# Kernel tuning notes

Hardware: AMD Instinct MI355X
Metric: run time of the kernel (lower is better)

Reference implementation:

```python
import jax, jax.numpy as jnp
import numpy as np

HEADS, OUT_CH = 8, 32  # GATConv(128, 256//8, heads=8) -> concat width 256
NEG_SLOPE = 0.2


def setup_inputs() -> dict:
    key = jax.random.key(0)
    ks = jax.random.split(key, 12)
    N, E, F_IN = 50000, 500000, 128
    H, C = HEADS, OUT_CH
    HID = H * C            # 256
    x = jax.random.normal(ks[0], (N, F_IN), dtype=jnp.float32)
    edge_index = jax.random.randint(ks[1], (2, E), 0, N, dtype=jnp.int64)
    s = 1.0 / np.sqrt(F_IN)
    W_gat = jax.random.normal(ks[2], (F_IN, H * C), dtype=jnp.float32) * s
    att_src = jax.random.normal(ks[3], (H, C), dtype=jnp.float32) * (1.0 / np.sqrt(C))
    att_dst = jax.random.normal(ks[4], (H, C), dtype=jnp.float32) * (1.0 / np.sqrt(C))
    b_gat = jnp.zeros((HID,), dtype=jnp.float32)
    W1 = jax.random.normal(ks[5], (HID, HID // 2), dtype=jnp.float32) * (1.0 / np.sqrt(HID))
    b1 = jnp.zeros((HID // 2,), dtype=jnp.float32)
    W2 = jax.random.normal(ks[6], (HID // 2, 6), dtype=jnp.float32) * (1.0 / np.sqrt(HID // 2))
    b2 = jnp.zeros((6,), dtype=jnp.float32)
    return {"x": x, "edge_index": edge_index, "W_gat": W_gat, "att_src": att_src,
            "att_dst": att_dst, "b_gat": b_gat, "W1": W1, "b1": b1, "W2": W2, "b2": b2}


def _gat_forward(x, edge_index, W_gat, att_src, att_dst, b_gat):
    N = x.shape[0]
    H, C = HEADS, OUT_CH
    # add self loops (PyG GATConv default)
    loop = jnp.arange(N, dtype=edge_index.dtype)
    src = jnp.concatenate([edge_index[0], loop])
    dst = jnp.concatenate([edge_index[1], loop])
    # per-node transform: [N, H, C]
    xh = (x @ W_gat).reshape(N, H, C)
    a_src = jnp.einsum('nhc,hc->nh', xh, att_src)  # [N, H]
    a_dst = jnp.einsum('nhc,hc->nh', xh, att_dst)  # [N, H]
    alpha = a_src[src] + a_dst[dst]                # [Etot, H]
    alpha = jnp.where(alpha >= 0, alpha, NEG_SLOPE * alpha)  # leaky relu
    # segment softmax over destination nodes
    m = jax.ops.segment_max(alpha, dst, num_segments=N)     # [N, H]
    m = jax.lax.stop_gradient(m)
    ex = jnp.exp(alpha - m[dst])
    denom = jax.ops.segment_sum(ex, dst, num_segments=N)    # [N, H]
    coef = ex / denom[dst]                                   # [Etot, H]
    # weighted scatter-add aggregation
    msgs = xh[src] * coef[:, :, None]                        # [Etot, H, C]
    out = jax.ops.segment_sum(msgs, dst, num_segments=N)     # [N, H, C]
    return out.reshape(N, H * C) + b_gat


def reference(x, edge_index, W_gat, att_src, att_dst, b_gat, W1, b1, W2, b2):
    h = _gat_forward(x, edge_index, W_gat, att_src, att_dst, b_gat)
    h = jax.nn.elu(h)
    g = jnp.mean(h, axis=0, keepdims=True)   # [1, 256] mean pool
    g = jax.nn.relu(g @ W1 + b1)
    return g @ W2 + b2                        # [1, 6] logits
```

## Files before the change

### kernel.cpp

```cpp
#include <hip/hip_runtime.h>
#include <hip/hip_fp8.h>
#include <math.h>

#define F_IN 128
#define HID 256
#define NH 8
#define CAP 40
#define BCAP 4096

typedef _Float16 h16;
typedef __attribute__((ext_vector_type(8))) _Float16 half8;
typedef __attribute__((ext_vector_type(4))) float f32x4;

__device__ inline unsigned char f32_to_fp8(float v) {
#if __has_builtin(__builtin_amdgcn_cvt_pk_fp8_f32)
    return (unsigned char)(__builtin_amdgcn_cvt_pk_fp8_f32(v, v, 0, false) & 0xff);
#else
    __hip_fp8_e4m3 t(v);
    return (unsigned char)t.__x;
#endif
}

__device__ inline void fp8x4_to_f32(int w, float* out) {
#if __has_builtin(__builtin_amdgcn_cvt_pk_f32_fp8)
    auto lo = __builtin_amdgcn_cvt_pk_f32_fp8(w, false);
    auto hi = __builtin_amdgcn_cvt_pk_f32_fp8(w, true);
    out[0] = lo[0]; out[1] = lo[1]; out[2] = hi[0]; out[3] = hi[1];
#else
    #pragma unroll
    for (int k = 0; k < 4; ++k) {
        __hip_fp8_e4m3 t;
        t.__x = (unsigned char)((w >> (8 * k)) & 0xff);
        out[k] = (float)t;
    }
#endif
}

__global__ void k_prep(const float* __restrict__ Wg,
                       const float* __restrict__ att_s,
                       const float* __restrict__ att_d,
                       h16* __restrict__ Wt_sw,
                       int* gcur, float* g2, int n) {
    int i = blockIdx.x * 256 + threadIdx.x;
    if (i < 256) gcur[i] = 0;
    if (i < 256 * HID) g2[i] = 0.f;
    if (i < 4352) {
        int fid = i;
        int lane16 = fid & 15;
        int quad = (fid >> 4) & 3;
        int ks = (fid >> 6) & 3;
        int ct = fid >> 8;
        int k0 = ks * 32 + quad * 8;
        half8 v;
        if (ct < 16) {
            int col = ct * 16 + lane16;
            #pragma unroll
            for (int j = 0; j < 8; ++j) v[j] = (h16)Wg[(size_t)(k0 + j) * HID + col];
        } else {
            const float* att = (lane16 < 8) ? att_s : att_d;
            int h = lane16 & 7;
            #pragma unroll
            for (int j = 0; j < 8; ++j) {
                float s = 0.f;
                for (int c = 0; c < 32; ++c)
                    s += Wg[(size_t)(k0 + j) * HID + h * 32 + c] * att[h * 32 + c];
                v[j] = (h16)s;
            }
        }
        *(half8*)(Wt_sw + (size_t)fid * 8) = v;
    }
}

__global__ __launch_bounds__(512) void k_ga(const float* __restrict__ x,
                                            const h16* __restrict__ Wt_sw,
                                            const int* __restrict__ dstp,
                                            const int* __restrict__ srcp,
                                            unsigned char* __restrict__ xh8,
                                            float* __restrict__ a_src,
                                            float* __restrict__ a_dst,
                                            unsigned int* __restrict__ gbuck,
                                            int* __restrict__ gcur,
                                            int n, int e, int ntiles,
                                            int nbuck, int npart) {
    __shared__ __align__(16) char smem[65536];
    int t = threadIdx.x;

    if (blockIdx.x < (unsigned)npart) {
        int* hist  = (int*)smem;
        int* scn   = hist + 256;
        int* lbase = scn + 256;
        int* lcur  = lbase + 256;
        int* base  = lcur + 256;
        unsigned int* sorted = (unsigned int*)(base + 256);
        int c0 = blockIdx.x * 2048;

        if (t < 256) hist[t] = 0;
        __syncthreads();

        unsigned int w4[4];
        int b4[4];
        #pragma unroll
        for (int k = 0; k < 4; ++k) {
            int i = c0 + k * 512 + t;
            if (i < e) {
                int d = dstp[i];
                int s = srcp[i];
                int b = d >> 8;
                b4[k] = b;
                w4[k] = ((unsigned)b << 24) | ((unsigned)(d & 255) << 16) | (unsigned)s;
                atomicAdd(&hist[b], 1);
            } else {
                b4[k] = -1;
                w4[k] = 0;
            }
        }
        __syncthreads();
        if (t < 256) scn[t] = hist[t];
        __syncthreads();
        for (int off = 1; off < 256; off <<= 1) {
            int u = 0;
            if (t < 256 && t >= off) u = scn[t - off];
            __syncthreads();
            if (t < 256 && t >= off) scn[t] += u;
            __syncthreads();
        }
        if (t < 256) {
            lbase[t] = scn[t] - hist[t];
            lcur[t] = 0;
            if (t < nbuck && hist[t] > 0) base[t] = atomicAdd(&gcur[t], hist[t]);
        }
        __syncthreads();
        #pragma unroll
        for (int k = 0; k < 4; ++k) {
            if (b4[k] >= 0) {
                int r = atomicAdd(&lcur[b4[k]], 1);
                sorted[lbase[b4[k]] + r] = w4[k];
            }
        }
        __syncthreads();
        int total = scn[255];
        for (int j = t; j < total; j += 512) {
            unsigned int w = sorted[j];
            int b = w >> 24;
            int addr = base[b] + (j - lbase[b]);
            if (addr < BCAP) gbuck[(size_t)b * BCAP + addr] = w;
        }
        return;
    }

    h16* wlds = (h16*)smem;
    int w = t >> 6, l = t & 63;
    int lane16 = l & 15, quad = l >> 4;

    float4 pv0[4], pv1[4];
    half8 bA[4];
    int tile = (blockIdx.x - npart) * 8 + w;
    bool have = tile < ntiles;
    int row0 = tile * 16;
    {
        const half8* wq = (const half8*)Wt_sw;
        #pragma unroll
        for (int ks = 0; ks < 4; ++ks) bA[ks] = wq[(64 + ks) * 64 + l];
    }
    if (have) {
        int rA = row0 + lane16;
        if (rA >= n) rA = n - 1;
        const float* xrow = x + (size_t)rA * F_IN + quad * 8;
        #pragma unroll
        for (int ks = 0; ks < 4; ++ks) {
            pv0[ks] = *(const float4*)(xrow + ks * 32);
            pv1[ks] = *(const float4*)(xrow + ks * 32 + 4);
        }
    }
    {
        const int4* wsrc = (const int4*)Wt_sw;
        int4* wdst = (int4*)wlds;
        #pragma unroll
        for (int i = 0; i < 8; ++i) wdst[i * 512 + t] = wsrc[i * 512 + t];
    }
    __syncthreads();
    if (!have) return;
    const h16* wl = wlds + (size_t)l * 8;

    half8 afr[4];
    #pragma unroll
    for (int ks = 0; ks < 4; ++ks) {
        half8 a;
        a[0] = (h16)pv0[ks].x; a[1] = (h16)pv0[ks].y;
        a[2] = (h16)pv0[ks].z; a[3] = (h16)pv0[ks].w;
        a[4] = (h16)pv1[ks].x; a[5] = (h16)pv1[ks].y;
        a[6] = (h16)pv1[ks].z; a[7] = (h16)pv1[ks].w;
        afr[ks] = a;
    }
    f32x4 acc[16];
    #pragma unroll
    for (int ct = 0; ct < 16; ++ct) acc[ct] = (f32x4){0.f, 0.f, 0.f, 0.f};
    #pragma unroll
    for (int ct = 0; ct < 16; ++ct) {
        #pragma unroll
        for (int ks = 0; ks < 4; ++ks) {
            half8 bfr = *(const half8*)(wl + (ct * 4 + ks) * 512);
            acc[ct] = __builtin_amdgcn_mfma_f32_16x16x32_f16(afr[ks], bfr, acc[ct], 0, 0, 0);
        }
    }
    f32x4 acc16 = (f32x4){0.f, 0.f, 0.f, 0.f};
    #pragma unroll
    for (int ks = 0; ks < 4; ++ks)
        acc16 = __builtin_amdgcn_mfma_f32_16x16x32_f16(afr[ks], bA[ks], acc16, 0, 0, 0);

    if (row0 + 16 <= n) {
        #pragma unroll
        for (int ct = 0; ct < 16; ++ct) {
            int col = ct * 16 + lane16;
            #pragma unroll
            for (int r = 0; r < 4; ++r)
                xh8[(size_t)(row0 + quad * 4 + r) * HID + col] = f32_to_fp8(acc[ct][r]);
        }
        float* ap = (lane16 < 8) ? a_src : a_dst;
        int h = lane16 & 7;
        #pragma unroll
        for (int r = 0; r < 4; ++r)
            ap[(row0 + quad * 4 + r) * NH + h] = acc16[r];
    } else {
        #pragma unroll
        for (int ct = 0; ct < 16; ++ct) {
            int col = ct * 16 + lane16;
            #pragma unroll
            for (int r = 0; r < 4; ++r) {
                int row = row0 + quad * 4 + r;
                if (row < n) xh8[(size_t)row * HID + col] = f32_to_fp8(acc[ct][r]);
            }
        }
        float* ap = (lane16 < 8) ? a_src : a_dst;
        int h = lane16 & 7;
        #pragma unroll
        for (int r = 0; r < 4; ++r) {
            int row = row0 + quad * 4 + r;
            if (row < n) ap[row * NH + h] = acc16[r];
        }
    }
}

__global__ __launch_bounds__(256) void k_bin(const unsigned int* __restrict__ gbuck,
                                             const int* __restrict__ gcur,
                                             int* __restrict__ cnt,
                                             unsigned short* __restrict__ bin,
                                             int n, int nbuck) {
    __shared__ int hist[256];
    __shared__ int cur[256];
    __shared__ __align__(16) unsigned short bl[256 * CAP];
    int t = threadIdx.x;
    int b = blockIdx.x;
    int count = gcur[b];
    if (count > BCAP) count = BCAP;
    hist[t] = 0;
    __syncthreads();
    const unsigned int* bb = gbuck + (size_t)b * BCAP;
    for (int j = t; j < count; j += 256) atomicAdd(&hist[(bb[j] >> 16) & 255], 1);
    __syncthreads();
    int node = b * 256 + t;
    if (node < n) {
        int hh = hist[t];
        cnt[node] = hh > CAP ? CAP : hh;
    }
    cur[t] = 0;
    __syncthreads();
    for (int j = t; j < count; j += 256) {
        unsigned int wv = bb[j];
        int dl = (wv >> 16) & 255;
        int pos = atomicAdd(&cur[dl], 1);
        if (pos < CAP) bl[dl * CAP + pos] = (unsigned short)(wv & 0xffff);
    }
    __syncthreads();
    const int4* s4 = (const int4*)bl;
    int4* d4 = (int4*)(bin + (size_t)b * 256 * CAP);
    #pragma unroll
    for (int q = 0; q < 5; ++q) d4[q * 256 + t] = s4[q * 256 + t];
}

__global__ __launch_bounds__(256) void k_agg(const unsigned char* __restrict__ xh8,
                                             const float* __restrict__ a_src,
                                             const float* __restrict__ a_dst,
                                             const int* __restrict__ cnt,
                                             const unsigned short* __restrict__ bin,
                                             const float* __restrict__ b_gat,
                                             float* __restrict__ g2, int n) {
    __shared__ float wpart[4][260];
    int t = threadIdx.x;
    int slot = t >> 4;
    int cl = t & 15;
    int c0 = cl * 16;
    int h = cl >> 1;
    int nn = blockIdx.x * 16 + slot;
    bool alive = nn < n;
    int nnc = alive ? nn : (n - 1);

    float ad = a_dst[nnc * NH + h];
    int deg = cnt[nnc];
    if (deg > CAP) deg = CAP;

    float al = a_src[nnc * NH + h] + ad;
    al = al > 0.f ? al : 0.2f * al;
    float ex = __expf(al);
    float den = ex;
    float acc[16];
    {
        int4 v = *(const int4*)(xh8 + (size_t)nnc * HID + c0);
        float f[16];
        fp8x4_to_f32(v.x, f); fp8x4_to_f32(v.y, f + 4);
        fp8x4_to_f32(v.z, f + 8); fp8x4_to_f32(v.w, f + 12);
        #pragma unroll
        for (int i = 0; i < 16; ++i) acc[i] = ex * f[i];
    }
    const unsigned short* brow = bin + (size_t)nnc * CAP;
    int j = 0;
    for (; j + 4 <= deg; j += 4) {
        ushort4 ss = *(const ushort4*)(brow + j);
        int s0 = ss.x, s1 = ss.y, s2 = ss.z, s3 = ss.w;
        float aa[4];
        aa[0] = a_src[s0 * NH + h];
        aa[1] = a_src[s1 * NH + h];
        aa[2] = a_src[s2 * NH + h];
        aa[3] = a_src[s3 * NH + h];
        int4 v0 = *(const int4*)(xh8 + (size_t)s0 * HID + c0);
        int4 v1 = *(const int4*)(xh8 + (size_t)s1 * HID + c0);
        int4 v2 = *(const int4*)(xh8 + (size_t)s2 * HID + c0);
        int4 v3 = *(const int4*)(xh8 + (size_t)s3 * HID + c0);
        float e4[4];
        #pragma unroll
        for (int q = 0; q < 4; ++q) {
            float a2 = aa[q] + ad;
            a2 = a2 > 0.f ? a2 : 0.2f * a2;
            e4[q] = __expf(a2);
            den += e4[q];
        }
        float f[16];
        fp8x4_to_f32(v0.x, f); fp8x4_to_f32(v0.y, f + 4);
        fp8x4_to_f32(v0.z, f + 8); fp8x4_to_f32(v0.w, f + 12);
        #pragma unroll
        for (int i = 0; i < 16; ++i) acc[i] += e4[0] * f[i];
        fp8x4_to_f32(v1.x, f); fp8x4_to_f32(v1.y, f + 4);
        fp8x4_to_f32(v1.z, f + 8); fp8x4_to_f32(v1.w, f + 12);
        #pragma unroll
        for (int i = 0; i < 16; ++i) acc[i] += e4[1] * f[i];
        fp8x4_to_f32(v2.x, f); fp8x4_to_f32(v2.y, f + 4);
        fp8x4_to_f32(v2.z, f + 8); fp8x4_to_f32(v2.w, f + 12);
        #pragma unroll
        for (int i = 0; i < 16; ++i) acc[i] += e4[2] * f[i];
        fp8x4_to_f32(v3.x, f); fp8x4_to_f32(v3.y, f + 4);
        fp8x4_to_f32(v3.z, f + 8); fp8x4_to_f32(v3.w, f + 12);
        #pragma unroll
        for (int i = 0; i < 16; ++i) acc[i] += e4[3] * f[i];
    }
    for (; j < deg; ++j) {
        int s = brow[j];
        float a2 = a_src[s * NH + h] + ad;
        a2 = a2 > 0.f ? a2 : 0.2f * a2;
        float e2 = __expf(a2);
        den += e2;
        int4 v = *(const int4*)(xh8 + (size_t)s * HID + c0);
        float f[16];
        fp8x4_to_f32(v.x, f); fp8x4_to_f32(v.y, f + 4);
        fp8x4_to_f32(v.z, f + 8); fp8x4_to_f32(v.w, f + 12);
        #pragma unroll
        for (int i = 0; i < 16; ++i) acc[i] += e2 * f[i];
    }
    float inv = 1.f / den;
    float val[16];
    #pragma unroll
    for (int q = 0; q < 4; ++q) {
        float4 bv = *(const float4*)(b_gat + c0 + q * 4);
        val[q * 4 + 0] = acc[q * 4 + 0] * inv + bv.x;
        val[q * 4 + 1] = acc[q * 4 + 1] * inv + bv.y;
        val[q * 4 + 2] = acc[q * 4 + 2] * inv + bv.z;
        val[q * 4 + 3] = acc[q * 4 + 3] * inv + bv.w;
    }
    #pragma unroll
    for (int i = 0; i < 16; ++i) {
        float v = val[i];
        v = v > 0.f ? v : expm1f(v);
        val[i] = alive ? v : 0.f;
    }
    #pragma unroll
    for (int i = 0; i < 16; ++i) {
        val[i] += __shfl_xor(val[i], 16, 64);
        val[i] += __shfl_xor(val[i], 32, 64);
    }
    int w = t >> 6, lw = t & 63;
    if (lw < 16) {
        #pragma unroll
        for (int q = 0; q < 4; ++q)
            *(f32x4*)(&wpart[w][c0 + q * 4]) =
                (f32x4){val[q * 4], val[q * 4 + 1], val[q * 4 + 2], val[q * 4 + 3]};
    }
    __syncthreads();
    float s = wpart[0][t] + wpart[1][t] + wpart[2][t] + wpart[3][t];
    atomicAdd(&g2[(blockIdx.x & 255) * HID + t], s);
}

__global__ __launch_bounds__(256) void k_mlp(const float* __restrict__ g2,
                                             const float* __restrict__ W1,
                                             const float* __restrict__ b1,
                                             const float* __restrict__ W2,
                                             const float* __restrict__ b2,
                                             float* __restrict__ out, int n) {
    __shared__ float gm[HID];
    __shared__ float h1p[2][128];
    __shared__ float h1[128];
    int t = threadIdx.x;
    float s = 0.f;
    for (int b = 0; b < 256; ++b) s += g2[b * HID + t];
    gm[t] = s / (float)n;
    __syncthreads();
    int o = t & 127, hf = t >> 7;
    float a = 0.f;
    #pragma unroll 4
    for (int k = hf * 128; k < hf * 128 + 128; ++k) a += gm[k] * W1[k * 128 + o];
    h1p[hf][o] = a;
    __syncthreads();
    if (t < 128) {
        float v = h1p[0][t] + h1p[1][t] + b1[t];
        h1[t] = v > 0.f ? v : 0.f;
    }
    __syncthreads();
    if (t < 6) {
        float a2 = b2[t];
        for (int k = 0; k < 128; ++k) a2 += h1[k] * W2[k * 6 + t];
        out[t] = a2;
    }
}

extern "C" void kernel_launch(void* const* d_in, const int* in_sizes, int n_in,
                              void* d_out, int out_size, void* d_ws, size_t ws_size,
                              hipStream_t stream) {
    const float* x     = (const float*)d_in[0];
    const int*   ei    = (const int*)d_in[1];
    const float* Wg    = (const float*)d_in[2];
    const float* att_s = (const float*)d_in[3];
    const float* att_d = (const float*)d_in[4];
    const float* b_gat = (const float*)d_in[5];
    const float* W1    = (const float*)d_in[6];
    const float* b1    = (const float*)d_in[7];
    const float* W2    = (const float*)d_in[8];
    const float* b2    = (const float*)d_in[9];

    int N = in_sizes[0] / F_IN;
    int E = in_sizes[1] / 2;
    const int* srcp = ei;
    const int* dstp = ei + E;
    int nblk = (N + 15) / 16;
    int ntiles = (N + 15) / 16;
    int nbuck = (N + 255) >> 8;

    char* ws = (char*)d_ws;
    size_t off = 0;
    auto alloc = [&](size_t bytes) {
        size_t o = off;
        off += (bytes + 255) & ~(size_t)255;
        return o;
    };
    unsigned char* xh8 = (unsigned char*)(ws + alloc((size_t)N * HID));
    h16*   Wt      = (h16*)(ws + alloc((size_t)4352 * 16));
    float* asr     = (float*)(ws + alloc((size_t)N * NH * 4));
    float* ads     = (float*)(ws + alloc((size_t)N * NH * 4));
    int*   cnt     = (int*)(ws + alloc((size_t)N * 4));
    unsigned short* bin = (unsigned short*)(ws + alloc((size_t)nbuck * 256 * CAP * 2));
    float* g2      = (float*)(ws + alloc((size_t)256 * HID * 4));
    unsigned int* gbuck = (unsigned int*)(ws + alloc((size_t)nbuck * BCAP * 4));
    int*   gcur    = (int*)(ws + alloc((size_t)256 * 4));

    int npart = (E + 2047) / 2048;
    int ngemm = (ntiles + 7) / 8;

    k_prep<<<256, 256, 0, stream>>>(Wg, att_s, att_d, Wt, gcur, g2, N);
    k_ga<<<npart + ngemm, 512, 0, stream>>>(x, Wt, dstp, srcp,
                                            xh8, asr, ads, gbuck, gcur,
                                            N, E, ntiles, nbuck, npart);
    k_bin<<<nbuck, 256, 0, stream>>>(gbuck, gcur, cnt, bin, N, nbuck);
    k_agg<<<nblk, 256, 0, stream>>>(xh8, asr, ads, cnt, bin, b_gat, g2, N);
    k_mlp<<<1, 256, 0, stream>>>(g2, W1, b1, W2, b2, (float*)d_out, N);
}
```

Measured before the change: 179.7 us.

## Interleave a_src into padded fp8 feature rows and stage GEMM stores through LDS

Each node's fp8 feature row is widened to a 288-byte stride, and its 8 a_src logits are stored inline after the 256 feature bytes. The gather in the aggregation kernel then reads the attention logit and the features from the same row, which removes a separate scattered a_src load per edge. The GEMM epilogue now writes fp8 results into LDS scratch first, then copies them out as coalesced 16-byte stores instead of byte-wise scattered writes. The cost is an extra block barrier, reuse of the weight LDS region as scratch, and a larger xh8 buffer.

Result: slower. 188.8 us (+5.0%).

```diff
diff --git a/kernel.cpp b/kernel.cpp
--- a/kernel.cpp
+++ b/kernel.cpp
@@ -7,6 +7,7 @@
 #define NH 8
 #define CAP 40
 #define BCAP 4096
+#define RSTRIDE 288
 
 typedef _Float16 h16;
 typedef __attribute__((ext_vector_type(8))) _Float16 half8;
@@ -76,7 +77,6 @@
                                             const int* __restrict__ dstp,
                                             const int* __restrict__ srcp,
                                             unsigned char* __restrict__ xh8,
-                                            float* __restrict__ a_src,
                                             float* __restrict__ a_dst,
                                             unsigned int* __restrict__ gbuck,
                                             int* __restrict__ gcur,
@@ -179,64 +179,68 @@
         for (int i = 0; i < 8; ++i) wdst[i * 512 + t] = wsrc[i * 512 + t];
     }
     __syncthreads();
+    const h16* wl = wlds + (size_t)l * 8;
+
+    f32x4 acc[16];
+    f32x4 acc16 = (f32x4){0.f, 0.f, 0.f, 0.f};
+    if (have) {
+        half8 afr[4];
+        #pragma unroll
+        for (int ks = 0; ks < 4; ++ks) {
+            half8 a;
+            a[0] = (h16)pv0[ks].x; a[1] = (h16)pv0[ks].y;
+            a[2] = (h16)pv0[ks].z; a[3] = (h16)pv0[ks].w;
+            a[4] = (h16)pv1[ks].x; a[5] = (h16)pv1[ks].y;
+            a[6] = (h16)pv1[ks].z; a[7] = (h16)pv1[ks].w;
+            afr[ks] = a;
+        }
+        #pragma unroll
+        for (int ct = 0; ct < 16; ++ct) acc[ct] = (f32x4){0.f, 0.f, 0.f, 0.f};
+        #pragma unroll
+        for (int ct = 0; ct < 16; ++ct) {
+            #pragma unroll
+            for (int ks = 0; ks < 4; ++ks) {
+                half8 bfr = *(const half8*)(wl + (ct * 4 + ks) * 512);
+                acc[ct] = __builtin_amdgcn_mfma_f32_16x16x32_f16(afr[ks], bfr, acc[ct], 0, 0, 0);
+            }
+        }
+        #pragma unroll
+        for (int ks = 0; ks < 4; ++ks)
+            acc16 = __builtin_amdgcn_mfma_f32_16x16x32_f16(afr[ks], bA[ks], acc16, 0, 0, 0);
+    }
+    __syncthreads();
     if (!have) return;
-    const h16* wl = wlds + (size_t)l * 8;
-
-    half8 afr[4];
-    #pragma unroll
-    for (int ks = 0; ks < 4; ++ks) {
-        half8 a;
-        a[0] = (h16)pv0[ks].x; a[1] = (h16)pv0[ks].y;
-        a[2] = (h16)pv0[ks].z; a[3] = (h16)pv0[ks].w;
-        a[4] = (h16)pv1[ks].x; a[5] = (h16)pv1[ks].y;
-        a[6] = (h16)pv1[ks].z; a[7] = (h16)pv1[ks].w;
-        afr[ks] = a;
-    }
-    f32x4 acc[16];
-    #pragma unroll
-    for (int ct = 0; ct < 16; ++ct) acc[ct] = (f32x4){0.f, 0.f, 0.f, 0.f};
+    unsigned char* scr = (unsigned char*)smem + (size_t)w * 4096;
     #pragma unroll
     for (int ct = 0; ct < 16; ++ct) {
         #pragma unroll
-        for (int ks = 0; ks < 4; ++ks) {
-            half8 bfr = *(const half8*)(wl + (ct * 4 + ks) * 512);
-            acc[ct] = __builtin_amdgcn_mfma_f32_16x16x32_f16(afr[ks], bfr, acc[ct], 0, 0, 0);
-        }
-    }
-    f32x4 acc16 = (f32x4){0.f, 0.f, 0.f, 0.f};
-    #pragma unroll
-    for (int ks = 0; ks < 4; ++ks)
-        acc16 = __builtin_amdgcn_mfma_f32_16x16x32_f16(afr[ks], bA[ks], acc16, 0, 0, 0);
-
-    if (row0 + 16 <= n) {
-        #pragma unroll
-        for (int ct = 0; ct < 16; ++ct) {
-            int col = ct * 16 + lane16;
+        for (int r = 0; r < 4; ++r)
+            scr[(quad * 4 + r) * 256 + ct * 16 + lane16] = f32_to_fp8(acc[ct][r]);
+    }
+    {
+        int rrow = l >> 2;
+        int chunk = (l & 3) * 16;
+        int grow = row0 + rrow;
+        if (grow < n) {
+            unsigned char* dst = xh8 + (size_t)grow * RSTRIDE;
             #pragma unroll
-            for (int r = 0; r < 4; ++r)
-                xh8[(size_t)(row0 + quad * 4 + r) * HID + col] = f32_to_fp8(acc[ct][r]);
-        }
-        float* ap = (lane16 < 8) ? a_src : a_dst;
-        int h = lane16 & 7;
-        #pragma unroll
-        for (int r = 0; r < 4; ++r)
-            ap[(row0 + quad * 4 + r) * NH + h] = acc16[r];
-    } else {
-        #pragma unroll
-        for (int ct = 0; ct < 16; ++ct) {
-            int col = ct * 16 + lane16;
-            #pragma unroll
-            for (int r = 0; r < 4; ++r) {
-                int row = row0 + quad * 4 + r;
-                if (row < n) xh8[(size_t)row * HID + col] = f32_to_fp8(acc[ct][r]);
-            }
-        }
-        float* ap = (lane16 < 8) ? a_src : a_dst;
-        int h = lane16 & 7;
+            for (int p = 0; p < 4; ++p)
+                *(int4*)(dst + p * 64 + chunk) =
+                    *(const int4*)(scr + rrow * 256 + p * 64 + chunk);
+        }
+    }
+    if (lane16 < 8) {
         #pragma unroll
         for (int r = 0; r < 4; ++r) {
             int row = row0 + quad * 4 + r;
-            if (row < n) ap[row * NH + h] = acc16[r];
+            if (row < n)
+                *(float*)(xh8 + (size_t)row * RSTRIDE + 256 + lane16 * 4) = acc16[r];
+        }
+    } else {
+        #pragma unroll
+        for (int r = 0; r < 4; ++r) {
+            int row = row0 + quad * 4 + r;
+            if (row < n) a_dst[row * NH + (lane16 - 8)] = acc16[r];
         }
     }
 }
@@ -279,7 +283,6 @@
 }
 
 __global__ __launch_bounds__(256) void k_agg(const unsigned char* __restrict__ xh8,
-                                             const float* __restrict__ a_src,
                                              const float* __restrict__ a_dst,
                                              const int* __restrict__ cnt,
                                              const unsigned short* __restrict__ bin,
@@ -299,13 +302,14 @@
     int deg = cnt[nnc];
     if (deg > CAP) deg = CAP;
 
-    float al = a_src[nnc * NH + h] + ad;
+    const unsigned char* rme = xh8 + (size_t)nnc * RSTRIDE;
+    float al = *(const float*)(rme + 256 + h * 4) + ad;
     al = al > 0.f ? al : 0.2f * al;
     float ex = __expf(al);
     float den = ex;
     float acc[16];
     {
-        int4 v = *(const int4*)(xh8 + (size_t)nnc * HID + c0);
+        int4 v = *(const int4*)(rme + c0);
         float f[16];
         fp8x4_to_f32(v.x, f); fp8x4_to_f32(v.y, f + 4);
         fp8x4_to_f32(v.z, f + 8); fp8x4_to_f32(v.w, f + 12);
@@ -316,16 +320,19 @@
     int j = 0;
     for (; j + 4 <= deg; j += 4) {
         ushort4 ss = *(const ushort4*)(brow + j);
-        int s0 = ss.x, s1 = ss.y, s2 = ss.z, s3 = ss.w;
+        const unsigned char* r0 = xh8 + (size_t)ss.x * RSTRIDE;
+        const unsigned char* r1 = xh8 + (size_t)ss.y * RSTRIDE;
+        const unsigned char* r2 = xh8 + (size_t)ss.z * RSTRIDE;
+        const unsigned char* r3 = xh8 + (size_t)ss.w * RSTRIDE;
         float aa[4];
-        aa[0] = a_src[s0 * NH + h];
-        aa[1] = a_src[s1 * NH + h];
-        aa[2] = a_src[s2 * NH + h];
-        aa[3] = a_src[s3 * NH + h];
-        int4 v0 = *(const int4*)(xh8 + (size_t)s0 * HID + c0);
-        int4 v1 = *(const int4*)(xh8 + (size_t)s1 * HID + c0);
-        int4 v2 = *(const int4*)(xh8 + (size_t)s2 * HID + c0);
-        int4 v3 = *(const int4*)(xh8 + (size_t)s3 * HID + c0);
+        aa[0] = *(const float*)(r0 + 256 + h * 4);
+        aa[1] = *(const float*)(r1 + 256 + h * 4);
+        aa[2] = *(const float*)(r2 + 256 + h * 4);
+        aa[3] = *(const float*)(r3 + 256 + h * 4);
+        int4 v0 = *(const int4*)(r0 + c0);
+        int4 v1 = *(const int4*)(r1 + c0);
+        int4 v2 = *(const int4*)(r2 + c0);
+        int4 v3 = *(const int4*)(r3 + c0);
         float e4[4];
         #pragma unroll
         for (int q = 0; q < 4; ++q) {
@@ -353,12 +360,12 @@
         for (int i = 0; i < 16; ++i) acc[i] += e4[3] * f[i];
     }
     for (; j < deg; ++j) {
-        int s = brow[j];
-        float a2 = a_src[s * NH + h] + ad;
+        const unsigned char* rs = xh8 + (size_t)brow[j] * RSTRIDE;
+        float a2 = *(const float*)(rs + 256 + h * 4) + ad;
         a2 = a2 > 0.f ? a2 : 0.2f * a2;
         float e2 = __expf(a2);
         den += e2;
-        int4 v = *(const int4*)(xh8 + (size_t)s * HID + c0);
+        int4 v = *(const int4*)(rs + c0);
         float f[16];
         fp8x4_to_f32(v.x, f); fp8x4_to_f32(v.y, f + 4);
         fp8x4_to_f32(v.z, f + 8); fp8x4_to_f32(v.w, f + 12);
@@ -459,9 +466,8 @@
         off += (bytes + 255) & ~(size_t)255;
         return o;
     };
-    unsigned char* xh8 = (unsigned char*)(ws + alloc((size_t)N * HID));
+    unsigned char* xh8 = (unsigned char*)(ws + alloc((size_t)N * RSTRIDE));
     h16*   Wt      = (h16*)(ws + alloc((size_t)4352 * 16));
-    float* asr     = (float*)(ws + alloc((size_t)N * NH * 4));
     float* ads     = (float*)(ws + alloc((size_t)N * NH * 4));
     int*   cnt     = (int*)(ws + alloc((size_t)N * 4));
     unsigned short* bin = (unsigned short*)(ws + alloc((size_t)nbuck * 256 * CAP * 2));
@@ -474,9 +480,9 @@
 
     k_prep<<<256, 256, 0, stream>>>(Wg, att_s, att_d, Wt, gcur, g2, N);
     k_ga<<<npart + ngemm, 512, 0, stream>>>(x, Wt, dstp, srcp,
-                                            xh8, asr, ads, gbuck, gcur,
+                                            xh8, ads, gbuck, gcur,
                                             N, E, ntiles, nbuck, npart);
     k_bin<<<nbuck, 256, 0, stream>>>(gbuck, gcur, cnt, bin, N, nbuck);
-    k_agg<<<nblk, 256, 0, stream>>>(xh8, asr, ads, cnt, bin, b_gat, g2, N);
+    k_agg<<<nblk, 256, 0, stream>>>(xh8, ads, cnt, bin, b_gat, g2, N);
     k_mlp<<<1, 256, 0, stream>>>(g2, W1, b1, W2, b2, (float*)d_out, N);
 }
```
